# Kernel optimization log

Measured on AMD Instinct MI355X. Metric: run time of the kernel, lower is better.

The kernel has to match this reference:

```python
import jax, jax.numpy as jnp
import numpy as np

N_NODES = 8192
N_PAIRS = 524288
MAX_PATH = 5
D_FEAT = 128


def setup_inputs() -> dict:
    key = jax.random.key(0)
    k_x, k_b, k_src, k_dst, k_len = jax.random.split(key, 5)
    x = jax.random.normal(k_x, (N_NODES, D_FEAT), dtype=jnp.float32)
    b = jax.random.normal(k_b, (MAX_PATH,), dtype=jnp.float32)
    src = jax.random.randint(k_src, (N_PAIRS,), 0, N_NODES, dtype=jnp.int32)
    dst = jax.random.randint(k_dst, (N_PAIRS,), 0, N_NODES, dtype=jnp.int32)
    path_len = jax.random.randint(k_len, (N_PAIRS,), 0, 10, dtype=jnp.int32)
    return {"x": x, "b": b, "src": src, "dst": dst, "path_len": path_len}


def reference(x, b, src, dst, path_len):
    # bucket index = min(len(path), max_path_distance) - 1, clipped into [0, MAX_PATH-1]
    bucket = jnp.clip(jnp.minimum(path_len, MAX_PATH) - 1, 0, MAX_PATH - 1)
    vals = b[bucket]  # [n_pairs] gather from tiny bias table
    num_nodes = x.shape[0]
    spatial_matrix = jnp.zeros((num_nodes, num_nodes), dtype=jnp.float32)
    # single batched scatter replaces the per-edge python loop
    spatial_matrix = spatial_matrix.at[src, dst].set(vals)
    return spatial_matrix
```

## Files before the change

### kernel.cpp

```cpp
#include <hip/hip_runtime.h>


#define N_NODES   8192
#define N_PAIRS   524288
#define MAX_PATH  5
#define NTHR      256
#define PER_THR   4
#define TBITS     20
#define TSIZE     (1u << TBITS)
#define TMASK     (TSIZE - 1u)

typedef unsigned long long u64;

__device__ __forceinline__ int bucket_of(int pl) {
    int b = min(pl, MAX_PATH) - 1;
    return max(0, min(b, MAX_PATH - 1));
}

__device__ __forceinline__ unsigned hash_cell(int cell) {
    return ((unsigned)cell * 2654435761u) >> (32 - TBITS);
}

__device__ __forceinline__ u64 pack_entry(int cell, int pri, int bkt) {
    return ((u64)(unsigned)pri << 29) | ((u64)(unsigned)cell << 3) | (unsigned)bkt;
}

__device__ __forceinline__ void table_insert(u64* T, int cell, int pri, int bkt) {
    unsigned h = hash_cell(cell);
    const u64 me = pack_entry(cell, pri, bkt);
    while (true) {
        u64 e = __hip_atomic_load(&T[h], __ATOMIC_RELAXED, __HIP_MEMORY_SCOPE_AGENT);
        if (e == 0ull) {
            u64 old = atomicCAS(&T[h], 0ull, me);
            if (old == 0ull) return;
            e = old;
        }
        if (((e >> 3) & 0x3FFFFFFull) == (u64)(unsigned)cell) {
            atomicMax(&T[h], me);
            return;
        }
        h = (h + 1) & TMASK;
    }
}

__global__ __launch_bounds__(NTHR) void scatter_pass(
        const int4* __restrict__ src4,
        const int4* __restrict__ dst4,
        const int4* __restrict__ plen4,
        u64* __restrict__ T) {
    const int t = blockIdx.x * NTHR + threadIdx.x;
    const int4 s = src4[t];
    const int4 d = dst4[t];
    const int4 p = plen4[t];
    const int base = t * PER_THR;

    table_insert(T, s.x * N_NODES + d.x, base + 1, bucket_of(p.x));
    table_insert(T, s.y * N_NODES + d.y, base + 2, bucket_of(p.y));
    table_insert(T, s.z * N_NODES + d.z, base + 3, bucket_of(p.z));
    table_insert(T, s.w * N_NODES + d.w, base + 4, bucket_of(p.w));
}

__global__ __launch_bounds__(NTHR) void resolve_pass(
        const int4* __restrict__ src4,
        const int4* __restrict__ dst4,
        const float* __restrict__ b,
        const u64* __restrict__ T,
        float* __restrict__ out_f) {
    const int t = blockIdx.x * NTHR + threadIdx.x;
    const int4 s = src4[t];
    const int4 d = dst4[t];
    const int base = t * PER_THR;

    const int cell[PER_THR] = { s.x * N_NODES + d.x, s.y * N_NODES + d.y,
                                s.z * N_NODES + d.z, s.w * N_NODES + d.w };
    #pragma unroll
    for (int k = 0; k < PER_THR; ++k) {
        unsigned h = hash_cell(cell[k]);
        u64 e;
        while (true) {
            e = T[h];
            if (e != 0ull &&
                ((e >> 3) & 0x3FFFFFFull) == (u64)(unsigned)cell[k]) break;
            h = (h + 1) & TMASK;
        }
        if ((int)(e >> 29) == base + k + 1) {
            __builtin_nontemporal_store(b[e & 7], &out_f[cell[k]]);
        }
    }
}

extern "C" void kernel_launch(void* const* d_in, const int* in_sizes, int n_in,
                              void* d_out, int out_size, void* d_ws, size_t ws_size,
                              hipStream_t stream) {
    const float* b    = (const float*)d_in[1];
    const int4* src4  = (const int4*)d_in[2];
    const int4* dst4  = (const int4*)d_in[3];
    const int4* plen4 = (const int4*)d_in[4];

    float* out_f = (float*)d_out;
    u64*   T     = (u64*)d_ws;

    hipMemsetAsync(d_ws, 0, (size_t)TSIZE * sizeof(u64), stream);

    const int blocks = N_PAIRS / (NTHR * PER_THR);

    scatter_pass<<<blocks, NTHR, 0, stream>>>(src4, dst4, plen4, T);
    resolve_pass<<<blocks, NTHR, 0, stream>>>(src4, dst4, b, T, out_f);
}
```

Baseline: 307.7 us.

## Resolve by streaming the hash table instead of re-probing per pair

```diff
diff --git a/kernel.cpp b/kernel.cpp
--- a/kernel.cpp
+++ b/kernel.cpp
@@ -26,16 +26,12 @@
 }
 
 __device__ __forceinline__ void table_insert(u64* T, int cell, int pri, int bkt) {
+    const u64 me = pack_entry(cell, pri, bkt);
     unsigned h = hash_cell(cell);
-    const u64 me = pack_entry(cell, pri, bkt);
     while (true) {
-        u64 e = __hip_atomic_load(&T[h], __ATOMIC_RELAXED, __HIP_MEMORY_SCOPE_AGENT);
-        if (e == 0ull) {
-            u64 old = atomicCAS(&T[h], 0ull, me);
-            if (old == 0ull) return;
-            e = old;
-        }
-        if (((e >> 3) & 0x3FFFFFFull) == (u64)(unsigned)cell) {
+        u64 old = atomicCAS(&T[h], 0ull, me);
+        if (old == 0ull) return;
+        if (((old >> 3) & 0x3FFFFFFull) == (u64)(unsigned)cell) {
             atomicMax(&T[h], me);
             return;
         }
@@ -61,30 +57,21 @@
 }
 
 __global__ __launch_bounds__(NTHR) void resolve_pass(
-        const int4* __restrict__ src4,
-        const int4* __restrict__ dst4,
+        const u64* __restrict__ T,
         const float* __restrict__ b,
-        const u64* __restrict__ T,
         float* __restrict__ out_f) {
     const int t = blockIdx.x * NTHR + threadIdx.x;
-    const int4 s = src4[t];
-    const int4 d = dst4[t];
-    const int base = t * PER_THR;
-
-    const int cell[PER_THR] = { s.x * N_NODES + d.x, s.y * N_NODES + d.y,
-                                s.z * N_NODES + d.z, s.w * N_NODES + d.w };
+    const ulonglong2* T2 = (const ulonglong2*)T;
     #pragma unroll
-    for (int k = 0; k < PER_THR; ++k) {
-        unsigned h = hash_cell(cell[k]);
-        u64 e;
-        while (true) {
-            e = T[h];
-            if (e != 0ull &&
-                ((e >> 3) & 0x3FFFFFFull) == (u64)(unsigned)cell[k]) break;
-            h = (h + 1) & TMASK;
+    for (int v = 0; v < 2; ++v) {
+        const ulonglong2 e2 = T2[t * 2 + v];
+        if (e2.x) {
+            const int cell = (int)((e2.x >> 3) & 0x3FFFFFFull);
+            __builtin_nontemporal_store(b[e2.x & 7], &out_f[cell]);
         }
-        if ((int)(e >> 29) == base + k + 1) {
-            __builtin_nontemporal_store(b[e & 7], &out_f[cell[k]]);
+        if (e2.y) {
+            const int cell = (int)((e2.y >> 3) & 0x3FFFFFFull);
+            __builtin_nontemporal_store(b[e2.y & 7], &out_f[cell]);
         }
     }
 }
@@ -102,8 +89,8 @@
 
     hipMemsetAsync(d_ws, 0, (size_t)TSIZE * sizeof(u64), stream);
 
-    const int blocks = N_PAIRS / (NTHR * PER_THR);
-
-    scatter_pass<<<blocks, NTHR, 0, stream>>>(src4, dst4, plen4, T);
-    resolve_pass<<<blocks, NTHR, 0, stream>>>(src4, dst4, b, T, out_f);
+    scatter_pass<<<N_PAIRS / (NTHR * PER_THR), NTHR, 0, stream>>>(
+        src4, dst4, plen4, T);
+    resolve_pass<<<TSIZE / (NTHR * PER_THR), NTHR, 0, stream>>>(
+        T, b, out_f);
 }
```

Measured after the change: 301.4 us. 2.0% less time.
